# Kernel tuning notes

Measured on AMD Instinct MI355X. Metric: run time of the kernel, lower is better.

## Reference

```python
import jax, jax.numpy as jnp
import numpy as np
import math

B, L, D = 4, 2048, 1024        # batch, x_len, x_dim
QKV, H = 64, 16                # qkv_dim, head_dim (number of heads)


def setup_inputs() -> dict:
    key = jax.random.key(0)
    ks = jax.random.split(key, 10)
    s = 1.0 / math.sqrt(D)
    return {
        "x": jax.random.normal(ks[0], (B, L, D), jnp.float32),
        "encoder_x": jax.random.normal(ks[1], (B, L, D), jnp.float32),
        "Wq": jax.random.normal(ks[2], (D, QKV * H), jnp.float32) * s,
        "bq": jax.random.normal(ks[3], (QKV * H,), jnp.float32) * 0.01,
        "Wk": jax.random.normal(ks[4], (D, QKV * H), jnp.float32) * s,
        "bk": jax.random.normal(ks[5], (QKV * H,), jnp.float32) * 0.01,
        "Wv": jax.random.normal(ks[6], (D, QKV * H), jnp.float32) * s,
        "bv": jax.random.normal(ks[7], (QKV * H,), jnp.float32) * 0.01,
        "Wo": jax.random.normal(ks[8], (QKV * H, D), jnp.float32) * s,
        "bo": jax.random.normal(ks[9], (D,), jnp.float32) * 0.01,
    }


def reference(x, encoder_x, Wq, bq, Wk, bk, Wv, bv, Wo, bo):
    # q,k from encoder_x; v from x  -> [B, L, H, QKV]
    q = (encoder_x @ Wq + bq).reshape(B, L, H, QKV)
    k = (encoder_x @ Wk + bk).reshape(B, L, H, QKV)
    v = (x @ Wv + bv).reshape(B, L, H, QKV)
    # explicit [B,H,L,L] score matrix + softmax over k (faithful to source)
    scores = jax.nn.softmax(
        jnp.einsum("bqhd,bkhd->bhqk", q, k) / math.sqrt(QKV), axis=-1
    )
    # faithful to source einsum 'bvhd,bhqk->bvhd': no shared contraction
    # index, so scores are summed over (q,k) and broadcast onto v per (b,h).
    attn = jnp.einsum("bvhd,bhqk->bvhd", v, scores).reshape(B, L, H * QKV)
    return attn @ Wo + bo
```

## Files before the change

### kernel.cpp

```cpp
#include <hip/hip_runtime.h>
#include <stdint.h>


typedef __attribute__((ext_vector_type(8))) short bf16x8;
typedef __attribute__((ext_vector_type(4))) float f32x4;

typedef __attribute__((address_space(1))) void as1_void;
typedef __attribute__((address_space(3))) void as3_void;
#define GLD16(g, s)                                                          \
  __builtin_amdgcn_global_load_lds((as1_void*)(g), (as3_void*)(s), 16, 0, 0)

__device__ __forceinline__ short f2bf(float f) {
  union { float f; uint32_t u; } v; v.f = f;
  uint32_t r = v.u + 0x7FFFu + ((v.u >> 16) & 1u);
  return (short)(r >> 16);
}

__device__ __forceinline__ bf16x8 pack8(f32x4 a, f32x4 b) {
  union { f32x4 f; uint32_t u[4]; } x, y;
  x.f = a; y.f = b;
#pragma unroll
  for (int t = 0; t < 4; ++t) x.u[t] += 0x8000u;
#pragma unroll
  for (int t = 0; t < 4; ++t) y.u[t] += 0x8000u;
  union { bf16x8 v; uint32_t u[4]; } o;
  o.u[0] = __builtin_amdgcn_perm(x.u[1], x.u[0], 0x07060302);
  o.u[1] = __builtin_amdgcn_perm(x.u[3], x.u[2], 0x07060302);
  o.u[2] = __builtin_amdgcn_perm(y.u[1], y.u[0], 0x07060302);
  o.u[3] = __builtin_amdgcn_perm(y.u[3], y.u[2], 0x07060302);
  return o.v;
}

__global__ __launch_bounds__(256) void wgemm(
    const float* __restrict__ Wo, const float* __restrict__ Wv,
    const float* __restrict__ bv, const float* __restrict__ bo,
    short* __restrict__ Wt, float* __restrict__ biasc) {
  constexpr int BK = 64, NW = 1024;
  __shared__ __align__(16) float Bsf[64 * BK];
  __shared__ __align__(16) float Ts[64 * 36];
  const int b = blockIdx.x, tid = threadIdx.x;

  if (b >= 512) {
    float* red = Bsf;
    const int b3 = b - 512;
    const int nx = tid & 15, ky = tid >> 4;
    const int n = b3 * 16 + nx;
    float s = 0.f;
    for (int k = ky; k < 1024; k += 16)
      s += bv[k] * Wo[(size_t)k * NW + n];
    red[tid] = s;
    __syncthreads();
#pragma unroll
    for (int st = 128; st >= 16; st >>= 1) {
      if (tid < st) red[tid] += red[tid + st];
      __syncthreads();
    }
    if (ky == 0) biasc[n] = 2048.0f * red[nx] + bo[n];
    return;
  }

  const int lane = tid & 63, wave = tid >> 6;
  const int bm = (b >> 4) * 32, bn = (b & 15) * 64;
  const int wm = (wave & 1) * 16, wn = (wave >> 1) * 32;
  const int l15 = lane & 15, quad = lane >> 4;

  f32x4 acc[2];
  acc[0] = (f32x4){0.f, 0.f, 0.f, 0.f};
  acc[1] = (f32x4){0.f, 0.f, 0.f, 0.f};

  const int br = tid >> 4, bc4 = (tid & 15) ^ (br & 7);
  const float* pb = Wv + (size_t)(bn + br) * NW + bc4 * 4;
  float* lb = Bsf + tid * 4;

  const int ajr = tid >> 3, ac4 = (tid & 7) * 4;
  const float* pa = Wo + (size_t)ajr * NW + bm + ac4;

  for (int kt = 0; kt < 1024; kt += BK) {
    float4 va = *(const float4*)(pa);
    float4 vb = *(const float4*)(pa + 32 * (size_t)NW);
    pa += (size_t)BK * NW;
#pragma unroll
    for (int s = 0; s < 4; ++s) GLD16(pb + (size_t)(16 * s) * NW, lb + 1024 * s);
    pb += BK;
    *(float4*)(Ts + ajr * 36 + ac4) = va;
    *(float4*)(Ts + (ajr + 32) * 36 + ac4) = vb;
    __syncthreads();
#pragma unroll
    for (int kk = 0; kk < 2; ++kk) {
      const float* tsp = Ts + ((kk * 4 + quad) * 8) * 36 + wm + l15;
      float av[8];
#pragma unroll
      for (int e = 0; e < 8; ++e) av[e] = tsp[e * 36];
      bf16x8 af = pack8((f32x4){av[0], av[1], av[2], av[3]},
                        (f32x4){av[4], av[5], av[6], av[7]});
#pragma unroll
      for (int j = 0; j < 2; ++j) {
        const int rn = wn + j * 16 + l15;
        const int c4 = kk * 8 + quad * 2;
        f32x4 u0 = *(const f32x4*)(Bsf + (rn * 16 + (c4 ^ (rn & 7))) * 4);
        f32x4 u1 = *(const f32x4*)(Bsf + (rn * 16 + ((c4 + 1) ^ (rn & 7))) * 4);
        acc[j] = __builtin_amdgcn_mfma_f32_16x16x32_bf16(af, pack8(u0, u1),
                                                         acc[j], 0, 0, 0);
      }
    }
    __syncthreads();
  }
#pragma unroll
  for (int j = 0; j < 2; ++j) {
    const int col = bn + wn + j * 16 + l15;
    const int row0 = bm + wm + quad * 4;
#pragma unroll
    for (int r = 0; r < 4; ++r)
      Wt[(size_t)(row0 + r) * NW + col] = f2bf(2048.f * acc[j][r]);
  }
}

__global__ __launch_bounds__(256, 4) void gemm_main(
    const float* __restrict__ X, const short* __restrict__ Bt,
    const float* __restrict__ bias, float* __restrict__ Out,
    int M, int N, int K) {
  constexpr int BK = 64;
  __shared__ __align__(16) char smem[32768];
  short* As0 = (short*)smem;
  short* As1 = (short*)(smem + 16384);
  const int tid = threadIdx.x, lane = tid & 63, wave = tid >> 6;
  const int b = blockIdx.x;
  const int bm = (b & 63) * 128;
  const int bn = (b >> 6) * 64;
  const int wm = (wave & 1) * 64, wn = (wave >> 1) * 32;
  const int l15 = lane & 15, quad = lane >> 4;

  f32x4 acc[4][2];
#pragma unroll
  for (int i = 0; i < 4; ++i)
#pragma unroll
    for (int j = 0; j < 2; ++j) acc[i][j] = (f32x4){0.f, 0.f, 0.f, 0.f};

  const int srow = tid >> 3, sc8 = (tid & 7) ^ (srow & 7);
  const float* pa = X + (size_t)(bm + srow) * K + sc8 * 8;
  short* la0 = As0 + tid * 8;
  short* la1 = As1 + tid * 8;

  const short* pb0 = Bt + (size_t)(bn + wn + l15) * K + quad * 8;
  const short* pb1 = pb0 + 16 * (size_t)K;

  float4 a0[4], a1[4];
  bf16x8 Bc[4], Bn[4];

#define LOADA(kt)                                                            \
  {                                                                          \
    _Pragma("unroll") for (int s = 0; s < 4; ++s) {                          \
      const float* p = pa + (size_t)(32 * s) * K + (kt);                     \
      a0[s] = *(const float4*)(p);                                           \
      a1[s] = *(const float4*)(p + 4);                                       \
    }                                                                        \
  }
#define LOADB(Br, kt)                                                        \
  {                                                                          \
    Br[0] = *(const bf16x8*)(pb0 + (kt));                                    \
    Br[1] = *(const bf16x8*)(pb1 + (kt));                                    \
    Br[2] = *(const bf16x8*)(pb0 + (kt) + 32);                               \
    Br[3] = *(const bf16x8*)(pb1 + (kt) + 32);                               \
  }
#define PACKWRITE(la)                                                        \
  {                                                                          \
    _Pragma("unroll") for (int s = 0; s < 4; ++s)                            \
        *(bf16x8*)((la) + 2048 * s) =                                        \
            pack8((f32x4){a0[s].x, a0[s].y, a0[s].z, a0[s].w},               \
                  (f32x4){a1[s].x, a1[s].y, a1[s].z, a1[s].w});              \
  }
#define COMPUTE(As, Br)                                                      \
  {                                                                          \
    _Pragma("unroll") for (int kk = 0; kk < 2; ++kk) {                       \
      bf16x8 af[4];                                                          \
      _Pragma("unroll") for (int i = 0; i < 4; ++i) {                        \
        const int r = wm + i * 16 + l15;                                     \
        af[i] =                                                              \
            *(const bf16x8*)((As) + r * BK + ((kk * 4 + quad) ^ (r & 7)) * 8);\
      }                                                                      \
      _Pragma("unroll") for (int i = 0; i < 4; ++i)                          \
          _Pragma("unroll") for (int j = 0; j < 2; ++j)                      \
              acc[i][j] = __builtin_amdgcn_mfma_f32_16x16x32_bf16(           \
                  af[i], Br[kk * 2 + j], acc[i][j], 0, 0, 0);                \
    }                                                                        \
  }

  LOADA(0);
  LOADB(Bc, 0);
  PACKWRITE(la0);
  __syncthreads();

  for (int trip = 0; trip < 8; ++trip) {
    const int kt_o = trip * 128 + 64;
    LOADA(kt_o);
    LOADB(Bn, kt_o);
    COMPUTE(As0, Bc);
    PACKWRITE(la1);
    __syncthreads();
    if (trip < 7) {
      const int kt_n = trip * 128 + 128;
      LOADA(kt_n);
      LOADB(Bc, kt_n);
      COMPUTE(As1, Bn);
      PACKWRITE(la0);
    } else {
      COMPUTE(As1, Bn);
    }
    __syncthreads();
  }
#undef LOADA
#undef LOADB
#undef PACKWRITE
#undef COMPUTE

  float* T = (float*)smem + wave * 576;
#pragma unroll
  for (int i = 0; i < 4; ++i) {
#pragma unroll
    for (int j = 0; j < 2; ++j) {
      const float bb = bias[bn + wn + j * 16 + l15];
#pragma unroll
      for (int r = 0; r < 4; ++r)
        T[(quad * 4 + r) * 36 + j * 16 + l15] = acc[i][j][r] + bb;
    }
#pragma unroll
    for (int c = 0; c < 2; ++c) {
      const int row = (lane >> 3) + 8 * c;
      f32x4 v = *(const f32x4*)(T + row * 36 + (lane & 7) * 4);
      *(f32x4*)(Out + (size_t)(bm + wm + i * 16 + row) * N + bn + wn +
                (lane & 7) * 4) = v;
    }
  }
}

extern "C" void kernel_launch(void* const* d_in, const int* in_sizes, int n_in,
                              void* d_out, int out_size, void* d_ws,
                              size_t ws_size, hipStream_t stream) {
  const float* x  = (const float*)d_in[0];
  const float* Wv = (const float*)d_in[6];
  const float* bv = (const float*)d_in[7];
  const float* Wo = (const float*)d_in[8];
  const float* bo = (const float*)d_in[9];
  float* out = (float*)d_out;

  constexpr int D = 1024, NO = 1024;
  constexpr int M = 8192;

  char* ws = (char*)d_ws;
  short* wt_bf = (short*)(ws);
  float* biasc = (float*)(ws + (2u << 20));

  wgemm<<<576, 256, 0, stream>>>(Wo, Wv, bv, bo, wt_bf, biasc);
  gemm_main<<<(M / 128) * (NO / 64), 256, 0, stream>>>(
      x, wt_bf, biasc, out, M, NO, D);
}
```

Before: 184.8 us.

## Widen main GEMM tile to 128x128 and stage B through LDS via direct loads

The output tile of the main GEMM grows from 128x64 to 128x128, so each wave computes 64x64 and the fp32 activation matrix X is re-read half as many times from global memory. B (the folded bf16 weight) is now copied into double-buffered swizzled LDS with global_load_lds, replacing per-wave register loads. The epilogue staging buffer is resized to match. Shared memory doubles to 64KB, the accumulator count doubles, and the occupancy hint is dropped, so fewer blocks fit per CU and the grid halves to 512 blocks.

```diff
diff --git a/kernel.cpp b/kernel.cpp
--- a/kernel.cpp
+++ b/kernel.cpp
@@ -115,37 +115,34 @@
   }
 }
 
-__global__ __launch_bounds__(256, 4) void gemm_main(
+__global__ __launch_bounds__(256) void gemm_main(
     const float* __restrict__ X, const short* __restrict__ Bt,
     const float* __restrict__ bias, float* __restrict__ Out,
     int M, int N, int K) {
   constexpr int BK = 64;
-  __shared__ __align__(16) char smem[32768];
+  __shared__ __align__(16) char smem[65536];
   short* As0 = (short*)smem;
   short* As1 = (short*)(smem + 16384);
+  short* Bs0 = (short*)(smem + 32768);
+  short* Bs1 = (short*)(smem + 49152);
   const int tid = threadIdx.x, lane = tid & 63, wave = tid >> 6;
   const int b = blockIdx.x;
   const int bm = (b & 63) * 128;
-  const int bn = (b >> 6) * 64;
-  const int wm = (wave & 1) * 64, wn = (wave >> 1) * 32;
+  const int bn = (b >> 6) * 128;
+  const int wm = (wave & 1) * 64, wn = (wave >> 1) * 64;
   const int l15 = lane & 15, quad = lane >> 4;
 
-  f32x4 acc[4][2];
+  f32x4 acc[4][4];
 #pragma unroll
   for (int i = 0; i < 4; ++i)
 #pragma unroll
-    for (int j = 0; j < 2; ++j) acc[i][j] = (f32x4){0.f, 0.f, 0.f, 0.f};
+    for (int j = 0; j < 4; ++j) acc[i][j] = (f32x4){0.f, 0.f, 0.f, 0.f};
 
   const int srow = tid >> 3, sc8 = (tid & 7) ^ (srow & 7);
   const float* pa = X + (size_t)(bm + srow) * K + sc8 * 8;
-  short* la0 = As0 + tid * 8;
-  short* la1 = As1 + tid * 8;
-
-  const short* pb0 = Bt + (size_t)(bn + wn + l15) * K + quad * 8;
-  const short* pb1 = pb0 + 16 * (size_t)K;
+  const short* pb = Bt + (size_t)(bn + srow) * K + sc8 * 8;
 
   float4 a0[4], a1[4];
-  bf16x8 Bc[4], Bn[4];
 
 #define LOADA(kt)                                                            \
   {                                                                          \
@@ -155,56 +152,59 @@
       a1[s] = *(const float4*)(p + 4);                                       \
     }                                                                        \
   }
-#define LOADB(Br, kt)                                                        \
-  {                                                                          \
-    Br[0] = *(const bf16x8*)(pb0 + (kt));                                    \
-    Br[1] = *(const bf16x8*)(pb1 + (kt));                                    \
-    Br[2] = *(const bf16x8*)(pb0 + (kt) + 32);                               \
-    Br[3] = *(const bf16x8*)(pb1 + (kt) + 32);                               \
-  }
-#define PACKWRITE(la)                                                        \
+#define LOADB(Bsx, kt)                                                       \
   {                                                                          \
     _Pragma("unroll") for (int s = 0; s < 4; ++s)                            \
-        *(bf16x8*)((la) + 2048 * s) =                                        \
+        GLD16(pb + (size_t)(32 * s) * K + (kt), (Bsx) + tid * 8 + 2048 * s); \
+  }
+#define PACKWRITE(Asx)                                                       \
+  {                                                                          \
+    _Pragma("unroll") for (int s = 0; s < 4; ++s)                            \
+        *(bf16x8*)((Asx) + tid * 8 + 2048 * s) =                             \
             pack8((f32x4){a0[s].x, a0[s].y, a0[s].z, a0[s].w},               \
                   (f32x4){a1[s].x, a1[s].y, a1[s].z, a1[s].w});              \
   }
-#define COMPUTE(As, Br)                                                      \
+#define COMPUTE(Asx, Bsx)                                                    \
   {                                                                          \
     _Pragma("unroll") for (int kk = 0; kk < 2; ++kk) {                       \
-      bf16x8 af[4];                                                          \
+      bf16x8 af[4], bfr[4];                                                  \
       _Pragma("unroll") for (int i = 0; i < 4; ++i) {                        \
         const int r = wm + i * 16 + l15;                                     \
-        af[i] =                                                              \
-            *(const bf16x8*)((As) + r * BK + ((kk * 4 + quad) ^ (r & 7)) * 8);\
+        af[i] = *(const bf16x8*)((Asx) + r * BK +                            \
+                                 ((kk * 4 + quad) ^ (r & 7)) * 8);           \
+      }                                                                      \
+      _Pragma("unroll") for (int j = 0; j < 4; ++j) {                        \
+        const int r = wn + j * 16 + l15;                                     \
+        bfr[j] = *(const bf16x8*)((Bsx) + r * BK +                           \
+                                  ((kk * 4 + quad) ^ (r & 7)) * 8);          \
       }                                                                      \
       _Pragma("unroll") for (int i = 0; i < 4; ++i)                          \
-          _Pragma("unroll") for (int j = 0; j < 2; ++j)                      \
+          _Pragma("unroll") for (int j = 0; j < 4; ++j)                      \
               acc[i][j] = __builtin_amdgcn_mfma_f32_16x16x32_bf16(           \
-                  af[i], Br[kk * 2 + j], acc[i][j], 0, 0, 0);                \
+                  af[i], bfr[j], acc[i][j], 0, 0, 0);                        \
     }                                                                        \
   }
 
   LOADA(0);
-  LOADB(Bc, 0);
-  PACKWRITE(la0);
+  LOADB(Bs0, 0);
+  PACKWRITE(As0);
   __syncthreads();
 
   for (int trip = 0; trip < 8; ++trip) {
     const int kt_o = trip * 128 + 64;
     LOADA(kt_o);
-    LOADB(Bn, kt_o);
-    COMPUTE(As0, Bc);
-    PACKWRITE(la1);
+    LOADB(Bs1, kt_o);
+    COMPUTE(As0, Bs0);
+    PACKWRITE(As1);
     __syncthreads();
     if (trip < 7) {
       const int kt_n = trip * 128 + 128;
       LOADA(kt_n);
-      LOADB(Bc, kt_n);
-      COMPUTE(As1, Bn);
-      PACKWRITE(la0);
+      LOADB(Bs0, kt_n);
+      COMPUTE(As1, Bs1);
+      PACKWRITE(As0);
     } else {
-      COMPUTE(As1, Bn);
+      COMPUTE(As1, Bs1);
     }
     __syncthreads();
   }
@@ -213,22 +213,23 @@
 #undef PACKWRITE
 #undef COMPUTE
 
-  float* T = (float*)smem + wave * 576;
+  float* T = (float*)smem + wave * 1088;
 #pragma unroll
   for (int i = 0; i < 4; ++i) {
 #pragma unroll
-    for (int j = 0; j < 2; ++j) {
+    for (int j = 0; j < 4; ++j) {
       const float bb = bias[bn + wn + j * 16 + l15];
 #pragma unroll
       for (int r = 0; r < 4; ++r)
-        T[(quad * 4 + r) * 36 + j * 16 + l15] = acc[i][j][r] + bb;
-    }
-#pragma unroll
-    for (int c = 0; c < 2; ++c) {
-      const int row = (lane >> 3) + 8 * c;
-      f32x4 v = *(const f32x4*)(T + row * 36 + (lane & 7) * 4);
+        T[(quad * 4 + r) * 68 + j * 16 + l15] = acc[i][j][r] + bb;
+    }
+#pragma unroll
+    for (int p = 0; p < 4; ++p) {
+      const int row = (lane >> 4) + 4 * p;
+      const int ch = lane & 15;
+      f32x4 v = *(const f32x4*)(T + row * 68 + ch * 4);
       *(f32x4*)(Out + (size_t)(bm + wm + i * 16 + row) * N + bn + wn +
-                (lane & 7) * 4) = v;
+                ch * 4) = v;
     }
   }
 }
@@ -251,6 +252,6 @@
   float* biasc = (float*)(ws + (2u << 20));
 
   wgemm<<<576, 256, 0, stream>>>(Wo, Wv, bv, bo, wt_bf, biasc);
-  gemm_main<<<(M / 128) * (NO / 64), 256, 0, stream>>>(
+  gemm_main<<<(M / 128) * (NO / 128), 256, 0, stream>>>(
       x, wt_bf, biasc, out, M, NO, D);
 }
```

Result: faster. 166.9 us (-9.7%).
